# Optimization experiments

Measured on AMD Instinct MI355X. Metric: run time of the kernel, lower is better.

Reference implementation:

```python
import jax, jax.numpy as jnp
import numpy as np

A, H, HI = 4, 3, 2  # nagents, n_pol_heads, n_intr_rew_heads (sep_extr_head=True)
# leave-one-out index table: row i lists all agents k != i, in ascending order (torch loop order)
LOO = np.array([[k for k in range(A) if k != i] for i in range(A)])  # [A, A-1]


def setup_inputs() -> dict:
    key = jax.random.key(0)
    ks = jax.random.split(key, 12)
    B, S, C, D = 32768, 256, 16, 128  # batch, vect_state_size, action_size, hidden_dim
    IN = C * (A - 1) + D  # 176 critic input dim
    r = lambda k, shp, s=0.05: jax.random.normal(k, shp, dtype=jnp.float32) * s
    return {
        "state_vect": jax.random.normal(ks[0], (B, S), dtype=jnp.float32),
        "acs": jax.random.normal(ks[1], (A, H, B, C), dtype=jnp.float32),
        "enc_W": r(ks[2], (S, D)),
        "enc_b": r(ks[3], (D,)),
        "extr_W1": r(ks[4], (H, A, IN, D)),
        "extr_b1": r(ks[5], (H, A, D)),
        "extr_W2": r(ks[6], (H, A, D, C)),
        "extr_b2": r(ks[7], (H, A, C)),
        "intr_W1": r(ks[8], (HI, A, IN, D)),
        "intr_b1": r(ks[9], (HI, A, D)),
        "intr_W2": r(ks[10], (HI, A, D, C)),
        "intr_b2": r(ks[11], (HI, A, C)),
    }


def reference(state_vect, acs, enc_W, enc_b, extr_W1, extr_b1, extr_W2, extr_b2,
              intr_W1, intr_b1, intr_W2, intr_b2):
    B, C = acs.shape[2], acs.shape[3]
    D = enc_W.shape[1]
    # shared state encoder: Linear -> ReLU
    enc = jax.nn.relu(state_vect @ enc_W + enc_b)  # [B, D]
    # leave-one-out action concat per (agent, head): cat(acs[k!=i, j]) ++ enc
    rel = acs[LOO]                                 # [A, A-1, H, B, C]
    rel = rel.transpose(0, 2, 3, 1, 4).reshape(A, H, B, (A - 1) * C)
    x = jnp.concatenate([rel, jnp.broadcast_to(enc, (A, H, B, D))], axis=-1)  # [A,H,B,IN]
    # greedy action index of agent i's own head-j policy output
    int_acs = jnp.argmax(acs, axis=-1)             # [A, H, B]

    def critic(xin, W1, b1, W2, b2):
        # xin: [A, Hc, B, IN]; W1: [Hc, A, IN, D]; W2: [Hc, A, D, C]
        h = jax.nn.relu(jnp.einsum('ahbi,haid->ahbd', xin, W1)
                        + b1.transpose(1, 0, 2)[:, :, None, :])
        return (jnp.einsum('ahbd,hadc->ahbc', h, W2)
                + b2.transpose(1, 0, 2)[:, :, None, :])  # [A, Hc, B, C]

    extr_all_q = critic(x, extr_W1, extr_b1, extr_W2, extr_b2)          # [A,H,B,C]
    extr_q = jnp.take_along_axis(extr_all_q, int_acs[..., None], axis=-1)  # [A,H,B,1]
    # intr critics exist only for heads j>=1 (sep_extr_head=True -> offset -1)
    intr_all_q = critic(x[:, 1:], intr_W1, intr_b1, intr_W2, intr_b2)   # [A,HI,B,C]
    intr_q = jnp.take_along_axis(intr_all_q, int_acs[:, 1:, :, None], axis=-1)  # [A,HI,B,1]
    return extr_q, intr_q
```

## Files before the change

### kernel.cpp

```cpp
#include <hip/hip_runtime.h>

#define NA 4
#define NH 3
#define NHI 2
#define Bsz 32768
#define Ssz 256
#define Csz 16
#define Dsz 128
#define INsz 176
#define NP 20
#define KP 192
#define GT 2

typedef __bf16 v8bf __attribute__((ext_vector_type(8)));
typedef float v4f __attribute__((ext_vector_type(4)));

#define OFF_ENC    0
#define OFF_ACSBF  8388608
#define OFF_W1F    20971520
#define OFF_ENCWF  21954560
#define OFF_W2T    22020096
#define OFF_AMX    22102016
#define OFF_ZERO   22495232

#define N_ACSROW (NA*NH*Bsz)
#define N_W1F   (NP*192*32)
#define N_ENCWF (256*32)
#define N_W2T   (NP*Csz*Dsz)
#define N_ZERO  16
#define N_PREP  (N_ACSROW+N_W1F+N_ENCWF+N_W2T+N_ZERO)

__global__ __launch_bounds__(256) void prep_kernel(
    const float* __restrict__ acs, const float* __restrict__ encW,
    const float* __restrict__ eW1, const float* __restrict__ iW1,
    const float* __restrict__ eW2, const float* __restrict__ iW2,
    const float* __restrict__ eb1, const float* __restrict__ ib1,
    char* __restrict__ ws)
{
    long tid = (long)blockIdx.x * 256 + threadIdx.x;

    if (tid < N_ACSROW) {
        const float4* src = (const float4*)(acs + (size_t)tid * 16);
        float4 f0 = src[0], f1 = src[1], f2 = src[2], f3 = src[3];
        float v[16] = {f0.x,f0.y,f0.z,f0.w, f1.x,f1.y,f1.z,f1.w,
                       f2.x,f2.y,f2.z,f2.w, f3.x,f3.y,f3.z,f3.w};
        v8bf o0, o1;
        #pragma unroll
        for (int i = 0; i < 8; ++i) { o0[i] = (__bf16)v[i]; o1[i] = (__bf16)v[8 + i]; }
        const int plane = (int)(tid >> 15);
        const int b     = (int)(tid & 32767);
        const int rt    = b >> 4, mm = b & 15;
        char* dstb = ws + OFF_ACSBF + (size_t)plane * 1048576 + (size_t)rt * 512 + mm * 16;
        *(v8bf*)dstb         = o0;
        *(v8bf*)(dstb + 256) = o1;
        float best = v[0]; int bi = 0;
        #pragma unroll
        for (int c = 1; c < 16; ++c) if (v[c] > best) { best = v[c]; bi = c; }
        ((unsigned char*)(ws + OFF_AMX))[tid] = (unsigned char)bi;
        return;
    }
    tid -= N_ACSROW;
    if (tid < N_W1F) {
        const int n4 = (int)(tid & 31) * 4;
        const int k  = (int)((tid >> 5) % 192);
        const int p  = (int)(tid / 6144);
        const float* W1; const float* B1;
        if (p < 12) { int ai = p / 3, hj = p % 3; int wi = hj * NA + ai;
                      W1 = eW1 + (size_t)wi * INsz * Dsz; B1 = eb1 + (size_t)wi * Dsz; }
        else { int qq = p - 12; int ai = qq >> 1, jj = qq & 1; int wi = jj * NA + ai;
               W1 = iW1 + (size_t)wi * INsz * Dsz; B1 = ib1 + (size_t)wi * Dsz; }
        float4 f;
        if (k < 128)        f = *(const float4*)(W1 + (size_t)(48 + k) * Dsz + n4);
        else if (k < INsz)  f = *(const float4*)(W1 + (size_t)(k - 128) * Dsz + n4);
        else if (k == INsz) f = *(const float4*)(B1 + n4);
        else                f = (float4){0.f, 0.f, 0.f, 0.f};
        const int kc = k >> 5, q = (k >> 3) & 3, j = k & 7;
        __bf16* dst = (__bf16*)(ws + OFF_W1F);
        const float fv[4] = {f.x, f.y, f.z, f.w};
        #pragma unroll
        for (int i = 0; i < 4; ++i) {
            const int n = n4 + i, nt = n >> 4, m = n & 15;
            dst[((size_t)(p * 6 + kc) * 8 + nt) * 512 + (q * 16 + m) * 8 + j] = (__bf16)fv[i];
        }
        return;
    }
    tid -= N_W1F;
    if (tid < N_ENCWF) {
        const int n4 = (int)(tid & 31) * 4;
        const int k  = (int)(tid >> 5);
        float4 f = *(const float4*)(encW + (size_t)k * Dsz + n4);
        const int kc = k >> 5, q = (k >> 3) & 3, j = k & 7;
        __bf16* dst = (__bf16*)(ws + OFF_ENCWF);
        const float fv[4] = {f.x, f.y, f.z, f.w};
        #pragma unroll
        for (int i = 0; i < 4; ++i) {
            const int n = n4 + i, nt = n >> 4, m = n & 15;
            dst[((size_t)kc * 8 + nt) * 512 + (q * 16 + m) * 8 + j] = (__bf16)fv[i];
        }
        return;
    }
    tid -= N_ENCWF;
    if (tid < N_W2T) {
        int d = (int)(tid & 127);
        int rest = (int)(tid >> 7);
        int c = rest & 15, p = rest >> 4;
        const float* W2;
        if (p < 12) { int ai = p / 3, hj = p % 3; W2 = eW2 + (size_t)(hj * NA + ai) * Dsz * Csz; }
        else { int qq = p - 12; int ai = qq >> 1, jj = qq & 1; W2 = iW2 + (size_t)(jj * NA + ai) * Dsz * Csz; }
        const int dlow = d & 15, dt = d >> 4;
        ((__bf16*)(ws + OFF_W2T))[(size_t)p * 2048 + c * 128 + ((dlow ^ c) * 8) + dt]
            = (__bf16)W2[(size_t)d * Csz + c];
        return;
    }
    tid -= N_W2T;
    if (tid < N_ZERO) {
        ((unsigned int*)(ws + OFF_ZERO))[tid] = (tid == 0) ? 0x00003F80u : 0u;
    }
}

__global__ __launch_bounds__(256) void enc_kernel(const float* __restrict__ sv,
                                                  const float* __restrict__ encb,
                                                  char* __restrict__ ws)
{
    __shared__ __bf16 svs[64][264];
    __shared__ __bf16 tb[4][16 * 136];

    const int t = threadIdx.x;
    const int wv = t >> 6, lane = t & 63, m = lane & 15, q = lane >> 4;
    const __bf16* encwf = (const __bf16*)(ws + OFF_ENCWF);
    char* enct = ws + OFF_ENC;

    {
        const float* src = sv + ((size_t)blockIdx.x * 64 + wv * 16) * Ssz;
        #pragma unroll
        for (int i = 0; i < 16; ++i) {
            float4 f = *(const float4*)(src + i * Ssz + lane * 4);
            __bf16* d = &svs[wv * 16 + i][lane * 4];
            d[0] = (__bf16)f.x; d[1] = (__bf16)f.y; d[2] = (__bf16)f.z; d[3] = (__bf16)f.w;
        }
    }

    v4f acc[8];
    #pragma unroll
    for (int nt = 0; nt < 8; ++nt) acc[nt] = (v4f){0.f, 0.f, 0.f, 0.f};

    #pragma unroll
    for (int kc = 0; kc < 8; ++kc) {
        v8bf af = *(const v8bf*)&svs[wv * 16 + m][kc * 32 + q * 8];
        #pragma unroll
        for (int nt = 0; nt < 8; ++nt) {
            v8bf bf = *(const v8bf*)(encwf + ((size_t)kc * 8 + nt) * 512 + lane * 8);
            acc[nt] = __builtin_amdgcn_mfma_f32_16x16x32_bf16(af, bf, acc[nt], 0, 0, 0);
        }
    }
    #pragma unroll
    for (int nt = 0; nt < 8; ++nt) {
        const float bias = encb[nt * 16 + m];
        #pragma unroll
        for (int rg = 0; rg < 4; ++rg) {
            float v = acc[nt][rg] + bias;
            v = v > 0.f ? v : 0.f;
            tb[wv][(q * 4 + rg) * 136 + nt * 16 + m] = (__bf16)v;
        }
    }
    const int rt = blockIdx.x * 4 + wv;
    #pragma unroll
    for (int kc = 0; kc < 4; ++kc) {
        v8bf v = *(const v8bf*)&tb[wv][m * 136 + kc * 32 + q * 8];
        *(v8bf*)(enct + ((size_t)(rt * 4 + kc) * 64 + lane) * 16) = v;
    }
}

#define LD_E(D, KC, GG) \
  { _Pragma("unroll") \
    for (int mt_ = 0; mt_ < 4; ++mt_) \
      D[mt_] = *(const v8bf*)(encL + (GG) * 65536 + mt_ * 4096 + (KC) * 1024); }

#define LD_4(D, GG) \
  { _Pragma("unroll") \
    for (int mt_ = 0; mt_ < 4; ++mt_) \
      D[mt_] = *(const v8bf*)(a4L + (GG) * 8192 + mt_ * 512); }

#define LD_5(D, GG) \
  { _Pragma("unroll") \
    for (int mt_ = 0; mt_ < 4; ++mt_) \
      D[mt_] = *(const v8bf*)(a5L + (GG) * g5 + mt_ * s5); }

#define MFMA_KC(AF, KC) \
  { __builtin_amdgcn_s_setprio(1); \
    _Pragma("unroll") \
    for (int nt_ = 0; nt_ < 8; ++nt_) { \
      v8bf bf_ = *(const v8bf*)&w1s[(size_t)(((KC) * 8 + nt_) * 512) + lane * 8]; \
      acc[0][nt_] = __builtin_amdgcn_mfma_f32_16x16x32_bf16(bf_, AF[0], acc[0][nt_], 0, 0, 0); \
      acc[1][nt_] = __builtin_amdgcn_mfma_f32_16x16x32_bf16(bf_, AF[1], acc[1][nt_], 0, 0, 0); \
      acc[2][nt_] = __builtin_amdgcn_mfma_f32_16x16x32_bf16(bf_, AF[2], acc[2][nt_], 0, 0, 0); \
      acc[3][nt_] = __builtin_amdgcn_mfma_f32_16x16x32_bf16(bf_, AF[3], acc[3][nt_], 0, 0, 0); \
    } \
    __builtin_amdgcn_s_setprio(0); }

__global__ __launch_bounds__(256, 2) void critic_kernel(
    const float* __restrict__ eb2, const float* __restrict__ ib2,
    const char* __restrict__ ws, float* __restrict__ out)
{
    __shared__ __bf16 w1s[6 * 8 * 512];
    __shared__ __bf16 w2s[16 * 128];
    __shared__ float  b2s[16];

    const int t = threadIdx.x;
    const int p  = blockIdx.y;
    const int rb = blockIdx.x;
    const int wv = t >> 6, lane = t & 63, m = lane & 15, q = lane >> 4;

    int ai, hj;
    const float* b2;
    float* outp;
    if (p < 12) {
        ai = p / 3; hj = p % 3;
        b2 = eb2 + (size_t)(hj * NA + ai) * Csz;
        outp = out + (size_t)(ai * NH + hj) * Bsz;
    } else {
        const int qq = p - 12; ai = qq >> 1; const int jj = qq & 1; hj = jj + 1;
        b2 = ib2 + (size_t)(jj * NA + ai) * Csz;
        outp = out + (size_t)NA * NH * Bsz + (size_t)(ai * NHI + jj) * Bsz;
    }

    const __bf16* w1f = (const __bf16*)(ws + OFF_W1F) + (size_t)p * 6 * 8 * 512;
    const __bf16* w2t = (const __bf16*)(ws + OFF_W2T) + (size_t)p * 2048;
    const unsigned char* amxp = (const unsigned char*)(ws + OFF_AMX)
        + (size_t)(ai * NH + hj) * Bsz + (size_t)rb * 512 + wv * 64;

    {
        const v8bf* src = (const v8bf*)w1f;
        #pragma unroll
        for (int i = 0; i < 12; ++i)
            ((v8bf*)w1s)[i * 256 + t] = src[i * 256 + t];
        ((v8bf*)w2s)[t] = ((const v8bf*)w2t)[t];
        if (t < 16) b2s[t] = b2[t];
    }

    const int loo0 = 0 + (0 >= ai), loo1 = 1 + (1 >= ai), loo2 = 2 + (2 >= ai);
    const int pA = loo0 * NH + hj, pB = loo1 * NH + hj, pC = loo2 * NH + hj;
    const int rtb = rb * 32 + wv * 4;
    const char* encL = ws + OFF_ENC + (size_t)rtb * 4096 + lane * 16;
    const size_t rtoff = (size_t)rtb * 512 + (lane & 31) * 16;
    const char* a4L = ws + OFF_ACSBF + (size_t)((q < 2) ? pA : pB) * 1048576 + rtoff;
    const char* a5L; int s5, g5;
    if (q < 2) { a5L = ws + OFF_ACSBF + (size_t)pC * 1048576 + rtoff; s5 = 512; g5 = 8192; }
    else       { a5L = ws + OFF_ZERO + (q - 2) * 16;                  s5 = 0;   g5 = 0;    }

    v4f acc[4][8];
    #pragma unroll
    for (int i = 0; i < 4; ++i)
        #pragma unroll
        for (int j = 0; j < 8; ++j)
            acc[i][j] = (v4f){0.f, 0.f, 0.f, 0.f};

    v8bf af0[4], af1[4], af2[4];
    LD_E(af0, 0, 0)
    LD_E(af1, 1, 0)

    __syncthreads();

    #pragma unroll
    for (int g = 0; g < GT; ++g) {
        LD_E(af2, 2, g)  MFMA_KC(af0, 0)
        LD_E(af0, 3, g)  MFMA_KC(af1, 1)
        LD_4(af1, g)     MFMA_KC(af2, 2)
        LD_5(af2, g)     MFMA_KC(af0, 3)
        if (g + 1 < GT) { LD_E(af0, 0, g + 1) }
        MFMA_KC(af1, 4)
        if (g + 1 < GT) { LD_E(af1, 1, g + 1) }
        MFMA_KC(af2, 5)

        int cb[4];
        #pragma unroll
        for (int mt = 0; mt < 4; ++mt)
            cb[mt] = amxp[g * 256 + mt * 16 + m];

        #pragma unroll
        for (int mt = 0; mt < 4; ++mt) {
            const int c = cb[mt];
            const __bf16* wcb = &w2s[c * 128];
            float s0 = 0.f, s1 = 0.f;
            #pragma unroll
            for (int rg = 0; rg < 4; rg += 2) {
                const v8bf wa = *(const v8bf*)&wcb[((q * 4 + rg) ^ c) * 8];
                const v8bf wb = *(const v8bf*)&wcb[((q * 4 + rg + 1) ^ c) * 8];
                #pragma unroll
                for (int nt = 0; nt < 8; ++nt) {
                    s0 += fmaxf(acc[mt][nt][rg],     0.f) * (float)wa[nt];
                    s1 += fmaxf(acc[mt][nt][rg + 1], 0.f) * (float)wb[nt];
                }
            }
            float tsum = s0 + s1;
            tsum += __shfl_xor(tsum, 16, 64);
            tsum += __shfl_xor(tsum, 32, 64);
            if (q == 0)
                outp[(size_t)rb * 512 + g * 256 + wv * 64 + mt * 16 + m] = tsum + b2s[c];
            if (g + 1 < GT) {
                #pragma unroll
                for (int nt = 0; nt < 8; ++nt) acc[mt][nt] = (v4f){0.f, 0.f, 0.f, 0.f};
            }
        }
    }
}

extern "C" void kernel_launch(void* const* d_in, const int* in_sizes, int n_in,
                              void* d_out, int out_size, void* d_ws, size_t ws_size,
                              hipStream_t stream) {
    const float* sv   = (const float*)d_in[0];
    const float* acs  = (const float*)d_in[1];
    const float* encW = (const float*)d_in[2];
    const float* encb = (const float*)d_in[3];
    const float* eW1  = (const float*)d_in[4];
    const float* eb1  = (const float*)d_in[5];
    const float* eW2  = (const float*)d_in[6];
    const float* eb2  = (const float*)d_in[7];
    const float* iW1  = (const float*)d_in[8];
    const float* ib1  = (const float*)d_in[9];
    const float* iW2  = (const float*)d_in[10];
    const float* ib2  = (const float*)d_in[11];
    float* out = (float*)d_out;
    char* ws = (char*)d_ws;

    hipLaunchKernelGGL(prep_kernel, dim3((N_PREP + 255) / 256), dim3(256), 0, stream,
                       acs, encW, eW1, iW1, eW2, iW2, eb1, ib1, ws);
    hipLaunchKernelGGL(enc_kernel, dim3(Bsz / 64), dim3(256), 0, stream, sv, encb, ws);
    hipLaunchKernelGGL(critic_kernel, dim3(Bsz / 512, NP), dim3(256), 0, stream,
                       eb2, ib2, ws, out);
}
```

Baseline: 150.3 us.

## Double rows per critic block, deepen A-fragment prefetch, and pack argmax indices

Each critic block now handles 1024 rows instead of 512 (GT 2→4), halving the grid so the per-block W1/W2 shared-memory staging is spread over more work. The main loop is manually unrolled with four rotating A-fragment register sets, so the loads for the next group's first three K-chunks are issued earlier and overlap the MFMA work. The prep kernel stores argmax indices transposed so each lane fetches its four indices with a single 32-bit load instead of four byte loads. In exchange, the extra fragment registers raise register pressure under the 2-blocks-per-CU launch bound, and the smaller grid of 640 blocks may not fill the GPU's compute units as evenly.

```diff
diff --git a/kernel.cpp b/kernel.cpp
--- a/kernel.cpp
+++ b/kernel.cpp
@@ -10,7 +10,7 @@
 #define INsz 176
 #define NP 20
 #define KP 192
-#define GT 2
+#define GT 4
 
 typedef __bf16 v8bf __attribute__((ext_vector_type(8)));
 typedef float v4f __attribute__((ext_vector_type(4)));
@@ -56,7 +56,9 @@
         float best = v[0]; int bi = 0;
         #pragma unroll
         for (int c = 1; c < 16; ++c) if (v[c] > best) { best = v[c]; bi = c; }
-        ((unsigned char*)(ws + OFF_AMX))[tid] = (unsigned char)bi;
+        const int grp = b >> 6, mt = (b >> 4) & 3, m = b & 15;
+        ((unsigned char*)(ws + OFF_AMX))[(size_t)plane * 32768 + grp * 64 + m * 4 + mt]
+            = (unsigned char)bi;
         return;
     }
     tid -= N_ACSROW;
@@ -198,6 +200,43 @@
     } \
     __builtin_amdgcn_s_setprio(0); }
 
+#define EPILOG(GG) \
+  { _Pragma("unroll") \
+    for (int mt = 0; mt < 4; ++mt) { \
+        const int c = (int)((cw >> (8 * mt)) & 255u); \
+        const __bf16* wcb = &w2s[c * 128]; \
+        float s0 = 0.f, s1 = 0.f; \
+        _Pragma("unroll") \
+        for (int rg = 0; rg < 4; rg += 2) { \
+            const v8bf wa = *(const v8bf*)&wcb[((q * 4 + rg) ^ c) * 8]; \
+            const v8bf wb = *(const v8bf*)&wcb[((q * 4 + rg + 1) ^ c) * 8]; \
+            _Pragma("unroll") \
+            for (int nt = 0; nt < 8; ++nt) { \
+                s0 += fmaxf(acc[mt][nt][rg],     0.f) * (float)wa[nt]; \
+                s1 += fmaxf(acc[mt][nt][rg + 1], 0.f) * (float)wb[nt]; \
+            } \
+        } \
+        float tsum = s0 + s1; \
+        tsum += __shfl_xor(tsum, 16, 64); \
+        tsum += __shfl_xor(tsum, 32, 64); \
+        if (q == 0) \
+            outp[(size_t)rb * 1024 + (GG) * 256 + wv * 64 + mt * 16 + m] = tsum + b2s[c]; \
+        if ((GG) + 1 < GT) { \
+            _Pragma("unroll") \
+            for (int nt = 0; nt < 8; ++nt) acc[mt][nt] = (v4f){0.f, 0.f, 0.f, 0.f}; \
+        } \
+    } }
+
+#define GBODY(GG, A_, B_, C_, D_, LAST) \
+  { const unsigned int cw = *(const unsigned int*)(amxL + (GG) * 256); \
+    LD_E(D_, 3, GG)                      MFMA_KC(A_, 0) \
+    LD_4(A_, GG)                         MFMA_KC(B_, 1) \
+    LD_5(B_, GG)                         MFMA_KC(C_, 2) \
+    if (!(LAST)) { LD_E(C_, 0, (GG)+1) } MFMA_KC(D_, 3) \
+    if (!(LAST)) { LD_E(D_, 1, (GG)+1) } MFMA_KC(A_, 4) \
+    if (!(LAST)) { LD_E(A_, 2, (GG)+1) } MFMA_KC(B_, 5) \
+    EPILOG(GG) }
+
 __global__ __launch_bounds__(256, 2) void critic_kernel(
     const float* __restrict__ eb2, const float* __restrict__ ib2,
     const char* __restrict__ ws, float* __restrict__ out)
@@ -226,8 +265,8 @@
 
     const __bf16* w1f = (const __bf16*)(ws + OFF_W1F) + (size_t)p * 6 * 8 * 512;
     const __bf16* w2t = (const __bf16*)(ws + OFF_W2T) + (size_t)p * 2048;
-    const unsigned char* amxp = (const unsigned char*)(ws + OFF_AMX)
-        + (size_t)(ai * NH + hj) * Bsz + (size_t)rb * 512 + wv * 64;
+    const char* amxL = ws + OFF_AMX + (size_t)(ai * NH + hj) * 32768
+        + ((size_t)rb * 16 + wv) * 64 + m * 4;
 
     {
         const v8bf* src = (const v8bf*)w1f;
@@ -240,7 +279,7 @@
 
     const int loo0 = 0 + (0 >= ai), loo1 = 1 + (1 >= ai), loo2 = 2 + (2 >= ai);
     const int pA = loo0 * NH + hj, pB = loo1 * NH + hj, pC = loo2 * NH + hj;
-    const int rtb = rb * 32 + wv * 4;
+    const int rtb = rb * 64 + wv * 4;
     const char* encL = ws + OFF_ENC + (size_t)rtb * 4096 + lane * 16;
     const size_t rtoff = (size_t)rtb * 512 + (lane & 31) * 16;
     const char* a4L = ws + OFF_ACSBF + (size_t)((q < 2) ? pA : pB) * 1048576 + rtoff;
@@ -255,54 +294,17 @@
         for (int j = 0; j < 8; ++j)
             acc[i][j] = (v4f){0.f, 0.f, 0.f, 0.f};
 
-    v8bf af0[4], af1[4], af2[4];
+    v8bf af0[4], af1[4], af2[4], af3[4];
     LD_E(af0, 0, 0)
     LD_E(af1, 1, 0)
+    LD_E(af2, 2, 0)
 
     __syncthreads();
 
-    #pragma unroll
-    for (int g = 0; g < GT; ++g) {
-        LD_E(af2, 2, g)  MFMA_KC(af0, 0)
-        LD_E(af0, 3, g)  MFMA_KC(af1, 1)
-        LD_4(af1, g)     MFMA_KC(af2, 2)
-        LD_5(af2, g)     MFMA_KC(af0, 3)
-        if (g + 1 < GT) { LD_E(af0, 0, g + 1) }
-        MFMA_KC(af1, 4)
-        if (g + 1 < GT) { LD_E(af1, 1, g + 1) }
-        MFMA_KC(af2, 5)
-
-        int cb[4];
-        #pragma unroll
-        for (int mt = 0; mt < 4; ++mt)
-            cb[mt] = amxp[g * 256 + mt * 16 + m];
-
-        #pragma unroll
-        for (int mt = 0; mt < 4; ++mt) {
-            const int c = cb[mt];
-            const __bf16* wcb = &w2s[c * 128];
-            float s0 = 0.f, s1 = 0.f;
-            #pragma unroll
-            for (int rg = 0; rg < 4; rg += 2) {
-                const v8bf wa = *(const v8bf*)&wcb[((q * 4 + rg) ^ c) * 8];
-                const v8bf wb = *(const v8bf*)&wcb[((q * 4 + rg + 1) ^ c) * 8];
-                #pragma unroll
-                for (int nt = 0; nt < 8; ++nt) {
-                    s0 += fmaxf(acc[mt][nt][rg],     0.f) * (float)wa[nt];
-                    s1 += fmaxf(acc[mt][nt][rg + 1], 0.f) * (float)wb[nt];
-                }
-            }
-            float tsum = s0 + s1;
-            tsum += __shfl_xor(tsum, 16, 64);
-            tsum += __shfl_xor(tsum, 32, 64);
-            if (q == 0)
-                outp[(size_t)rb * 512 + g * 256 + wv * 64 + mt * 16 + m] = tsum + b2s[c];
-            if (g + 1 < GT) {
-                #pragma unroll
-                for (int nt = 0; nt < 8; ++nt) acc[mt][nt] = (v4f){0.f, 0.f, 0.f, 0.f};
-            }
-        }
-    }
+    GBODY(0, af0, af1, af2, af3, 0)
+    GBODY(1, af2, af3, af0, af1, 0)
+    GBODY(2, af0, af1, af2, af3, 0)
+    GBODY(3, af2, af3, af0, af1, 1)
 }
 
 extern "C" void kernel_launch(void* const* d_in, const int* in_sizes, int n_in,
@@ -326,6 +328,6 @@
     hipLaunchKernelGGL(prep_kernel, dim3((N_PREP + 255) / 256), dim3(256), 0, stream,
                        acs, encW, eW1, iW1, eW2, iW2, eb1, ib1, ws);
     hipLaunchKernelGGL(enc_kernel, dim3(Bsz / 64), dim3(256), 0, stream, sv, encb, ws);
-    hipLaunchKernelGGL(critic_kernel, dim3(Bsz / 512, NP), dim3(256), 0, stream,
+    hipLaunchKernelGGL(critic_kernel, dim3(Bsz / 1024, NP), dim3(256), 0, stream,
                        eb2, ib2, ws, out);
 }
```

Result: slower. 160.6 us (+6.8%).
